# Kernel optimization log

Hardware: AMD Instinct MI355X
Metric: run time of the kernel (lower is better)

Reference implementation:

```python
import jax, jax.numpy as jnp
import numpy as np

N_NODES = 100000
N_EDGES = 1600000
NUM_FEATURES = 512
HIDDEN = 128
NUM_CLASSES = 40


def setup_inputs() -> dict:
    key = jax.random.key(0)
    ks = jax.random.split(key, 6)
    x = jax.random.normal(ks[0], (N_NODES, NUM_FEATURES), dtype=jnp.float32)
    edge_index = jax.random.randint(ks[1], (2, N_EDGES), 0, N_NODES, dtype=jnp.int32)
    W1 = jax.random.normal(ks[2], (NUM_FEATURES, HIDDEN), dtype=jnp.float32) * 0.05
    b1 = jnp.zeros((HIDDEN,), dtype=jnp.float32)
    W2 = jax.random.normal(ks[3], (HIDDEN, NUM_CLASSES), dtype=jnp.float32) * 0.05
    b2 = jnp.zeros((NUM_CLASSES,), dtype=jnp.float32)
    return {"x": x, "edge_index": edge_index, "W1": W1, "b1": b1, "W2": W2, "b2": b2}


def _gcn_conv(x, W, b, src, dst, n):
    # PyG GCNConv: h = W x; out = D^{-1/2} (A + I) D^{-1/2} h + b
    h = x @ W                                            # [N, out]
    deg = jax.ops.segment_sum(jnp.ones(src.shape[0], h.dtype), dst,
                              num_segments=n) + 1.0      # +1 for self loop
    inv_sqrt = jax.lax.rsqrt(deg)                        # [N]
    coef = inv_sqrt[src] * inv_sqrt[dst]                 # [E]
    msgs = h[src] * coef[:, None]                        # [E, out] gather
    agg = jax.ops.segment_sum(msgs, dst, num_segments=n) # scatter-add
    agg = agg + h * (inv_sqrt * inv_sqrt)[:, None]       # self-loop term
    return agg + b


def reference(x, edge_index, W1, b1, W2, b2):
    src, dst = edge_index[0], edge_index[1]
    n = x.shape[0]
    h = jax.nn.relu(_gcn_conv(x, W1, b1, src, dst, n))
    # F.dropout(training=self.training): eval mode -> identity
    out = _gcn_conv(h, W2, b2, src, dst, n)
    return jax.nn.log_softmax(out, axis=1)
```

## Files before the change

kernel.cpp:

```cpp
#include <hip/hip_runtime.h>
#include <hip/hip_bf16.h>
#include <math.h>

#define N_NODES 100000
#define N_EDGES 1600000
#define F_IN 512
#define HID 128
#define NCLS 40

typedef __attribute__((ext_vector_type(8))) short short8;
typedef __attribute__((ext_vector_type(4))) float floatx4;

__device__ __forceinline__ unsigned short f2bf(float x) {
    unsigned u = __builtin_bit_cast(unsigned, x);
    unsigned r = (u + 0x7FFFu + ((u >> 16) & 1u)) >> 16;
    return (unsigned short)r;
}
__device__ __forceinline__ float bflo(unsigned u) {
    return __builtin_bit_cast(float, u << 16);
}
__device__ __forceinline__ float bfhi(unsigned u) {
    return __builtin_bit_cast(float, u & 0xFFFF0000u);
}


__global__ void k_zero_int(int* p, int n) {
    int i = blockIdx.x * blockDim.x + threadIdx.x;
    if (i < n) p[i] = 0;
}


__global__ void k_count_deg(const int* __restrict__ dst, int* __restrict__ deg, int e) {
    int i = blockIdx.x * blockDim.x + threadIdx.x;
    if (i < e) atomicAdd(&deg[dst[i]], 1);
}


#define SCAN_B 256

__global__ __launch_bounds__(SCAN_B) void k_scan1(const int* __restrict__ deg,
                                                  int* __restrict__ rp,
                                                  int* __restrict__ bsums,
                                                  float* __restrict__ inv, int n) {
    __shared__ int s[SCAN_B];
    int tid = threadIdx.x;
    int i = blockIdx.x * SCAN_B + tid;
    int v = (i < n) ? deg[i] : 0;
    if (i < n) inv[i] = rsqrtf((float)v + 1.0f);
    s[tid] = v;
    __syncthreads();
    for (int off = 1; off < SCAN_B; off <<= 1) {
        int t = (tid >= off) ? s[tid - off] : 0;
        __syncthreads();
        s[tid] += t;
        __syncthreads();
    }
    if (i < n) rp[i] = s[tid] - v;
    if (tid == SCAN_B - 1) bsums[blockIdx.x] = s[tid];
}

__global__ __launch_bounds__(512) void k_scan2(int* __restrict__ bsums, int nb) {
    __shared__ int s[512];
    int tid = threadIdx.x;
    int v = (tid < nb) ? bsums[tid] : 0;
    s[tid] = v;
    __syncthreads();
    for (int off = 1; off < 512; off <<= 1) {
        int t = (tid >= off) ? s[tid - off] : 0;
        __syncthreads();
        s[tid] += t;
        __syncthreads();
    }
    if (tid < nb) bsums[tid] = s[tid] - v;
}

__global__ void k_scan3(int* __restrict__ rp, const int* __restrict__ bsums, int n) {
    int i = blockIdx.x * SCAN_B + threadIdx.x;
    if (i < n) rp[i] += bsums[blockIdx.x];
}


__global__ void k_fill(const int* __restrict__ src, const int* __restrict__ dst,
                       const int* __restrict__ rp, int* __restrict__ cursor,
                       int* __restrict__ csr_src, int e) {
    int i = blockIdx.x * blockDim.x + threadIdx.x;
    if (i >= e) return;
    int d = dst[i];
    int pos = atomicAdd(&cursor[d], 1);
    csr_src[rp[d] + pos] = src[i];
}


__global__ __launch_bounds__(256) void k_w1t(const float* __restrict__ W1,
                                             unsigned short* __restrict__ W1t) {
    int idx = blockIdx.x * 256 + threadIdx.x;
    int n = idx >> 9, k = idx & 511;
    W1t[idx] = f2bf(W1[k * HID + n]);
}


__global__ __launch_bounds__(256) void k_w2prep(const float* __restrict__ W2,
                                                unsigned short* __restrict__ W2th,
                                                unsigned short* __restrict__ W2tl) {
    int idx = blockIdx.x * 256 + threadIdx.x;
    int n = idx >> 7, k = idx & 127;
    float v = (n < NCLS) ? W2[k * NCLS + n] : 0.f;
    unsigned short hi = f2bf(v);
    unsigned short lo = f2bf(v - bflo(hi));
    W2th[idx] = hi;
    W2tl[idx] = lo;
}


#define GM 128

__global__ __launch_bounds__(256) void k_gemm1_mfma(
    const float* __restrict__ A,
    const unsigned short* __restrict__ Bt,
    const float* __restrict__ inv,
    unsigned short* __restrict__ C,
    int M)
{
    __shared__ unsigned short Asl[128 * 40];
    __shared__ unsigned short Bsl[128 * 40];

    const int tid  = threadIdx.x;
    const int wave = tid >> 6;
    const int lane = tid & 63;
    const int quad = lane >> 4;
    const int l15  = lane & 15;
    const int wm   = (wave >> 1) * 64;
    const int wn   = (wave & 1) * 64;
    const int block_m = blockIdx.x * GM;

    floatx4 acc[4][4];
    #pragma unroll
    for (int i = 0; i < 4; ++i)
        #pragma unroll
        for (int j = 0; j < 4; ++j) acc[i][j] = (floatx4){0.f, 0.f, 0.f, 0.f};

    for (int k0 = 0; k0 < F_IN; k0 += 32) {
        #pragma unroll
        for (int i = 0; i < 4; ++i) {
            int f  = tid + 256 * i;
            int r  = f >> 3;
            int kq = f & 7;
            int gr = block_m + r;
            gr = gr < M ? gr : M - 1;
            floatx4 v = *(const floatx4*)&A[(size_t)gr * F_IN + k0 + kq * 4];
            unsigned lo = (unsigned)f2bf(v.x) | ((unsigned)f2bf(v.y) << 16);
            unsigned hi = (unsigned)f2bf(v.z) | ((unsigned)f2bf(v.w) << 16);
            *(uint2*)&Asl[r * 40 + kq * 4] = make_uint2(lo, hi);
        }
        #pragma unroll
        for (int i = 0; i < 2; ++i) {
            int f  = tid + 256 * i;
            int r  = f >> 2;
            int kq = f & 3;
            int4 v = *(const int4*)&Bt[(size_t)r * F_IN + k0 + kq * 8];
            *(int4*)&Bsl[r * 40 + kq * 8] = v;
        }
        __syncthreads();

        short8 af[4], bf[4];
        #pragma unroll
        for (int t = 0; t < 4; ++t)
            af[t] = *(const short8*)&Asl[(wm + t * 16 + l15) * 40 + quad * 8];
        #pragma unroll
        for (int t = 0; t < 4; ++t)
            bf[t] = *(const short8*)&Bsl[(wn + t * 16 + l15) * 40 + quad * 8];

        #pragma unroll
        for (int tm = 0; tm < 4; ++tm)
            #pragma unroll
            for (int tn = 0; tn < 4; ++tn)
                acc[tm][tn] = __builtin_amdgcn_mfma_f32_16x16x32_bf16(
                    af[tm], bf[tn], acc[tm][tn], 0, 0, 0);
        __syncthreads();
    }

    #pragma unroll
    for (int tm = 0; tm < 4; ++tm) {
        #pragma unroll
        for (int r = 0; r < 4; ++r) {
            int row = block_m + wm + tm * 16 + quad * 4 + r;
            if (row < M) {
                float iv = inv[row];
                #pragma unroll
                for (int tn = 0; tn < 4; ++tn)
                    C[(size_t)row * HID + wn + tn * 16 + l15] =
                        f2bf(acc[tm][tn][r] * iv);
            }
        }
    }
}


__global__ __launch_bounds__(256) void k_gather1(
    const unsigned* __restrict__ h1s,
    const int* __restrict__ rp, const int* __restrict__ deg,
    const float* __restrict__ inv, const int* __restrict__ csr_src,
    const float* __restrict__ b1, float* __restrict__ hrelu)
{
    const int wave = threadIdx.x >> 6;
    const int lane = threadIdx.x & 63;
    const int node = blockIdx.x * 4 + wave;
    const int start = rp[node];
    const int cnt = deg[node];

    unsigned u = h1s[(size_t)node * 64 + lane];
    float acc0 = bflo(u), acc1 = bfhi(u);

    int t = 0;
    for (; t + 4 <= cnt; t += 4) {
        int s0 = csr_src[start + t + 0];
        int s1 = csr_src[start + t + 1];
        int s2 = csr_src[start + t + 2];
        int s3 = csr_src[start + t + 3];
        unsigned u0 = h1s[(size_t)s0 * 64 + lane];
        unsigned u1 = h1s[(size_t)s1 * 64 + lane];
        unsigned u2 = h1s[(size_t)s2 * 64 + lane];
        unsigned u3 = h1s[(size_t)s3 * 64 + lane];
        acc0 += (bflo(u0) + bflo(u1)) + (bflo(u2) + bflo(u3));
        acc1 += (bfhi(u0) + bfhi(u1)) + (bfhi(u2) + bfhi(u3));
    }
    for (; t < cnt; ++t) {
        int s = csr_src[start + t];
        unsigned uu = h1s[(size_t)s * 64 + lane];
        acc0 += bflo(uu);
        acc1 += bfhi(uu);
    }

    float invd = inv[node];
    float2 b = *(const float2*)&b1[lane * 2];
    float v0 = fmaxf(acc0 * invd + b.x, 0.f);
    float v1 = fmaxf(acc1 * invd + b.y, 0.f);
    *(float2*)&hrelu[(size_t)node * HID + lane * 2] = make_float2(v0, v1);
}


#define G2M 128

__global__ __launch_bounds__(256) void k_gemm2_mfma(
    const float* __restrict__ H,
    const unsigned short* __restrict__ Bh,
    const unsigned short* __restrict__ Bl,
    const float* __restrict__ inv,
    unsigned short* __restrict__ C,
    int M)
{
    __shared__ unsigned short Ahs[128 * 40];
    __shared__ unsigned short Als[128 * 40];
    __shared__ unsigned short Bhs[48 * 136];
    __shared__ unsigned short Bls[48 * 136];

    const int tid  = threadIdx.x;
    const int wave = tid >> 6;
    const int lane = tid & 63;
    const int quad = lane >> 4;
    const int l15  = lane & 15;
    const int wm   = wave * 32;
    const int block_m = blockIdx.x * G2M;

    for (int i = tid; i < 768; i += 256) {
        int n = i >> 4;
        int k = (i & 15) * 8;
        *(int4*)&Bhs[n * 136 + k] = *(const int4*)&Bh[n * 128 + k];
        *(int4*)&Bls[n * 136 + k] = *(const int4*)&Bl[n * 128 + k];
    }

    floatx4 acc[2][3];
    #pragma unroll
    for (int i = 0; i < 2; ++i)
        #pragma unroll
        for (int j = 0; j < 3; ++j) acc[i][j] = (floatx4){0.f, 0.f, 0.f, 0.f};

    for (int k0 = 0; k0 < HID; k0 += 32) {
        #pragma unroll
        for (int i = 0; i < 4; ++i) {
            int f  = tid + 256 * i;
            int r  = f >> 3;
            int kq = f & 7;
            int gr = block_m + r;
            gr = gr < M ? gr : M - 1;
            floatx4 v = *(const floatx4*)&H[(size_t)gr * HID + k0 + kq * 4];
            unsigned short hx = f2bf(v.x), hy = f2bf(v.y);
            unsigned short hz = f2bf(v.z), hw = f2bf(v.w);
            unsigned short lx = f2bf(v.x - bflo(hx));
            unsigned short ly = f2bf(v.y - bflo(hy));
            unsigned short lz = f2bf(v.z - bflo(hz));
            unsigned short lw = f2bf(v.w - bflo(hw));
            *(uint2*)&Ahs[r * 40 + kq * 4] =
                make_uint2((unsigned)hx | ((unsigned)hy << 16),
                           (unsigned)hz | ((unsigned)hw << 16));
            *(uint2*)&Als[r * 40 + kq * 4] =
                make_uint2((unsigned)lx | ((unsigned)ly << 16),
                           (unsigned)lz | ((unsigned)lw << 16));
        }
        __syncthreads();

        short8 ah[2], al[2], bh[3], bl[3];
        #pragma unroll
        for (int t = 0; t < 2; ++t) {
            ah[t] = *(const short8*)&Ahs[(wm + t * 16 + l15) * 40 + quad * 8];
            al[t] = *(const short8*)&Als[(wm + t * 16 + l15) * 40 + quad * 8];
        }
        #pragma unroll
        for (int t = 0; t < 3; ++t) {
            bh[t] = *(const short8*)&Bhs[(t * 16 + l15) * 136 + k0 + quad * 8];
            bl[t] = *(const short8*)&Bls[(t * 16 + l15) * 136 + k0 + quad * 8];
        }

        #pragma unroll
        for (int tm = 0; tm < 2; ++tm)
            #pragma unroll
            for (int tn = 0; tn < 3; ++tn) {
                acc[tm][tn] = __builtin_amdgcn_mfma_f32_16x16x32_bf16(
                    ah[tm], bh[tn], acc[tm][tn], 0, 0, 0);
                acc[tm][tn] = __builtin_amdgcn_mfma_f32_16x16x32_bf16(
                    al[tm], bh[tn], acc[tm][tn], 0, 0, 0);
                acc[tm][tn] = __builtin_amdgcn_mfma_f32_16x16x32_bf16(
                    ah[tm], bl[tn], acc[tm][tn], 0, 0, 0);
            }
        __syncthreads();
    }

    #pragma unroll
    for (int tm = 0; tm < 2; ++tm) {
        #pragma unroll
        for (int r = 0; r < 4; ++r) {
            int row = block_m + wm + tm * 16 + quad * 4 + r;
            if (row < M) {
                float iv = inv[row];
                #pragma unroll
                for (int tn = 0; tn < 3; ++tn) {
                    int col = tn * 16 + l15;
                    if (col < NCLS)
                        C[(size_t)row * NCLS + col] = f2bf(acc[tm][tn][r] * iv);
                }
            }
        }
    }
}


__global__ __launch_bounds__(256) void k_gather2(
    const unsigned* __restrict__ h2s,
    const int* __restrict__ rp, const int* __restrict__ deg,
    const float* __restrict__ inv, const int* __restrict__ csr_src,
    const float* __restrict__ b2, float* __restrict__ out)
{
    const int wave = threadIdx.x >> 6;
    const int lane = threadIdx.x & 63;
    const int node = blockIdx.x * 4 + wave;
    const int g = lane / 20;
    const int j = lane - g * 20;
    const int start = rp[node];
    const int cnt = deg[node];

    float acc0 = 0.f, acc1 = 0.f;
    if (g == 0) {
        unsigned u = h2s[(size_t)node * 20 + j];
        acc0 = bflo(u);
        acc1 = bfhi(u);
    }
    if (g < 3) {
        int t = g;
        for (; t + 3 < cnt; t += 6) {
            int s0 = csr_src[start + t];
            int s1 = csr_src[start + t + 3];
            unsigned u0 = h2s[(size_t)s0 * 20 + j];
            unsigned u1 = h2s[(size_t)s1 * 20 + j];
            acc0 += bflo(u0) + bflo(u1);
            acc1 += bfhi(u0) + bfhi(u1);
        }
        if (t < cnt) {
            int s = csr_src[start + t];
            unsigned u = h2s[(size_t)s * 20 + j];
            acc0 += bflo(u);
            acc1 += bfhi(u);
        }
    }
    acc0 += __shfl(acc0, j + 20) + __shfl(acc0, j + 40);
    acc1 += __shfl(acc1, j + 20) + __shfl(acc1, j + 40);

    float invd = inv[node];
    float v0 = -INFINITY, v1 = -INFINITY;
    if (g == 0) {
        float2 b = *(const float2*)&b2[j * 2];
        v0 = acc0 * invd + b.x;
        v1 = acc1 * invd + b.y;
    }
    float m = fmaxf(v0, v1);
    #pragma unroll
    for (int mask = 16; mask; mask >>= 1) m = fmaxf(m, __shfl_xor(m, mask));
    float e = (g == 0) ? (__expf(v0 - m) + __expf(v1 - m)) : 0.f;
    #pragma unroll
    for (int mask = 16; mask; mask >>= 1) e += __shfl_xor(e, mask);
    if (g == 0) {
        float lg = __logf(e);
        *(float2*)&out[(size_t)node * NCLS + j * 2] =
            make_float2(v0 - m - lg, v1 - m - lg);
    }
}


extern "C" void kernel_launch(void* const* d_in, const int* in_sizes, int n_in,
                              void* d_out, int out_size, void* d_ws, size_t ws_size,
                              hipStream_t stream) {
    const float* x   = (const float*)d_in[0];
    const int*   ei  = (const int*)d_in[1];
    const float* W1  = (const float*)d_in[2];
    const float* b1  = (const float*)d_in[3];
    const float* W2  = (const float*)d_in[4];
    const float* b2  = (const float*)d_in[5];
    float* out = (float*)d_out;

    const int* src = ei;
    const int* dst = ei + N_EDGES;

    char* wsb = (char*)d_ws;
    float* inv      = (float*)wsb;
    float* slot1    = inv + 131072;
    float* hrelu    = slot1 + (size_t)N_NODES * HID;
    int*   deg      = (int*)(hrelu + (size_t)N_NODES * HID);
    int*   rp       = deg + 131072;
    int*   cursor   = rp + 131072;
    int*   bsums    = cursor + 131072;
    int*   csr_src  = bsums + 1024;
    unsigned short* W2th = (unsigned short*)(csr_src + N_EDGES);
    unsigned short* W2tl = W2th + 48 * 128;
    unsigned short* h1s_st = (unsigned short*)slot1;
    unsigned short* h2s_st = (unsigned short*)slot1;
    unsigned* h1s_ld = (unsigned*)slot1;
    unsigned* h2s_ld = (unsigned*)slot1;
    unsigned short* W1t = (unsigned short*)cursor;

    const int T = 256;
    const int NB = (N_NODES + SCAN_B - 1) / SCAN_B;

    k_zero_int<<<(131072 * 2) / T, T, 0, stream>>>(deg, 131072 * 2);
    k_zero_int<<<131072 / T, T, 0, stream>>>(cursor, 131072);
    k_count_deg<<<N_EDGES / T, T, 0, stream>>>(dst, deg, N_EDGES);

    k_scan1<<<NB, SCAN_B, 0, stream>>>(deg, rp, bsums, inv, N_NODES);
    k_scan2<<<1, 512, 0, stream>>>(bsums, NB);
    k_scan3<<<NB, SCAN_B, 0, stream>>>(rp, bsums, N_NODES);
    k_fill<<<N_EDGES / T, T, 0, stream>>>(src, dst, rp, cursor, csr_src, N_EDGES);

    k_w1t<<<(F_IN * HID) / T, T, 0, stream>>>(W1, W1t);
    k_w2prep<<<(48 * 128) / T, T, 0, stream>>>(W2, W2th, W2tl);

    k_gemm1_mfma<<<(N_NODES + GM - 1) / GM, T, 0, stream>>>(x, W1t, inv, h1s_st, N_NODES);
    k_gather1<<<N_NODES / 4, T, 0, stream>>>(h1s_ld, rp, deg, inv, csr_src, b1, hrelu);

    k_gemm2_mfma<<<(N_NODES + G2M - 1) / G2M, T, 0, stream>>>(hrelu, W2th, W2tl, inv, h2s_st, N_NODES);
    k_gather2<<<N_NODES / 4, T, 0, stream>>>(h2s_ld, rp, deg, inv, csr_src, b2, out);
}
```

Measured before the change: 625.6 us.

## Double-buffer LDS and prefetch global tiles in both GEMM kernels

The first GEMM now uses two LDS buffers and issues the global loads for the next K-slice into registers before running the MFMAs on the current slice. The converted values go to the alternate buffer afterwards, which leaves one barrier per step. The second GEMM prefetches its next H slice into registers after the barrier, so the loads overlap the MFMA work. This is meant to hide global load latency, at the cost of twice the LDS and more registers, which could lower occupancy.

```diff
diff --git a/kernel.cpp b/kernel.cpp
--- a/kernel.cpp
+++ b/kernel.cpp
@@ -121,8 +121,8 @@
     unsigned short* __restrict__ C,
     int M)
 {
-    __shared__ unsigned short Asl[128 * 40];
-    __shared__ unsigned short Bsl[128 * 40];
+    __shared__ unsigned short Asl[2][128 * 40];
+    __shared__ unsigned short Bsl[2][128 * 40];
 
     const int tid  = threadIdx.x;
     const int wave = tid >> 6;
@@ -133,49 +133,85 @@
     const int wn   = (wave & 1) * 64;
     const int block_m = blockIdx.x * GM;
 
+    const int ra = tid >> 3, kqa = tid & 7;
+    const int rb = tid >> 2, kqb = tid & 3;
+
+    size_t aoff[4];
+    #pragma unroll
+    for (int i = 0; i < 4; ++i) {
+        int gr = block_m + ra + 32 * i;
+        gr = gr < M ? gr : M - 1;
+        aoff[i] = (size_t)gr * F_IN + kqa * 4;
+    }
+    size_t boff[2];
+    #pragma unroll
+    for (int i = 0; i < 2; ++i)
+        boff[i] = (size_t)(rb + 64 * i) * F_IN + kqb * 8;
+
+    floatx4 areg[4];
+    int4 breg[2];
+
     floatx4 acc[4][4];
     #pragma unroll
     for (int i = 0; i < 4; ++i)
         #pragma unroll
         for (int j = 0; j < 4; ++j) acc[i][j] = (floatx4){0.f, 0.f, 0.f, 0.f};
 
-    for (int k0 = 0; k0 < F_IN; k0 += 32) {
-        #pragma unroll
-        for (int i = 0; i < 4; ++i) {
-            int f  = tid + 256 * i;
-            int r  = f >> 3;
-            int kq = f & 7;
-            int gr = block_m + r;
-            gr = gr < M ? gr : M - 1;
-            floatx4 v = *(const floatx4*)&A[(size_t)gr * F_IN + k0 + kq * 4];
-            unsigned lo = (unsigned)f2bf(v.x) | ((unsigned)f2bf(v.y) << 16);
-            unsigned hi = (unsigned)f2bf(v.z) | ((unsigned)f2bf(v.w) << 16);
-            *(uint2*)&Asl[r * 40 + kq * 4] = make_uint2(lo, hi);
-        }
-        #pragma unroll
-        for (int i = 0; i < 2; ++i) {
-            int f  = tid + 256 * i;
-            int r  = f >> 2;
-            int kq = f & 3;
-            int4 v = *(const int4*)&Bt[(size_t)r * F_IN + k0 + kq * 8];
-            *(int4*)&Bsl[r * 40 + kq * 8] = v;
-        }
-        __syncthreads();
-
-        short8 af[4], bf[4];
+    #pragma unroll
+    for (int i = 0; i < 4; ++i) areg[i] = *(const floatx4*)&A[aoff[i]];
+    #pragma unroll
+    for (int i = 0; i < 2; ++i) breg[i] = *(const int4*)&Bt[boff[i]];
+    #pragma unroll
+    for (int i = 0; i < 4; ++i) {
+        floatx4 v = areg[i];
+        unsigned lo = (unsigned)f2bf(v.x) | ((unsigned)f2bf(v.y) << 16);
+        unsigned hi = (unsigned)f2bf(v.z) | ((unsigned)f2bf(v.w) << 16);
+        *(uint2*)&Asl[0][(ra + 32 * i) * 40 + kqa * 4] = make_uint2(lo, hi);
+    }
+    #pragma unroll
+    for (int i = 0; i < 2; ++i)
+        *(int4*)&Bsl[0][(rb + 64 * i) * 40 + kqb * 8] = breg[i];
+    __syncthreads();
+
+    #pragma unroll 2
+    for (int step = 0; step < 16; ++step) {
+        const int buf = step & 1;
+
+        if (step < 15) {
+            const int k1 = (step + 1) * 32;
+            #pragma unroll
+            for (int i = 0; i < 4; ++i) areg[i] = *(const floatx4*)&A[aoff[i] + k1];
+            #pragma unroll
+            for (int i = 0; i < 2; ++i) breg[i] = *(const int4*)&Bt[boff[i] + k1];
+        }
+
+        short8 af[4], bfr[4];
         #pragma unroll
         for (int t = 0; t < 4; ++t)
-            af[t] = *(const short8*)&Asl[(wm + t * 16 + l15) * 40 + quad * 8];
+            af[t] = *(const short8*)&Asl[buf][(wm + t * 16 + l15) * 40 + quad * 8];
         #pragma unroll
         for (int t = 0; t < 4; ++t)
-            bf[t] = *(const short8*)&Bsl[(wn + t * 16 + l15) * 40 + quad * 8];
+            bfr[t] = *(const short8*)&Bsl[buf][(wn + t * 16 + l15) * 40 + quad * 8];
 
         #pragma unroll
         for (int tm = 0; tm < 4; ++tm)
             #pragma unroll
             for (int tn = 0; tn < 4; ++tn)
                 acc[tm][tn] = __builtin_amdgcn_mfma_f32_16x16x32_bf16(
-                    af[tm], bf[tn], acc[tm][tn], 0, 0, 0);
+                    af[tm], bfr[tn], acc[tm][tn], 0, 0, 0);
+
+        if (step < 15) {
+            #pragma unroll
+            for (int i = 0; i < 4; ++i) {
+                floatx4 v = areg[i];
+                unsigned lo = (unsigned)f2bf(v.x) | ((unsigned)f2bf(v.y) << 16);
+                unsigned hi = (unsigned)f2bf(v.z) | ((unsigned)f2bf(v.w) << 16);
+                *(uint2*)&Asl[buf ^ 1][(ra + 32 * i) * 40 + kqa * 4] = make_uint2(lo, hi);
+            }
+            #pragma unroll
+            for (int i = 0; i < 2; ++i)
+                *(int4*)&Bsl[buf ^ 1][(rb + 64 * i) * 40 + kqb * 8] = breg[i];
+        }
         __syncthreads();
     }
 
@@ -269,36 +305,51 @@
         *(int4*)&Bls[n * 136 + k] = *(const int4*)&Bl[n * 128 + k];
     }
 
+    const int ra = tid >> 3, kqa = tid & 7;
+    size_t aoff[4];
+    #pragma unroll
+    for (int i = 0; i < 4; ++i) {
+        int gr = block_m + ra + 32 * i;
+        gr = gr < M ? gr : M - 1;
+        aoff[i] = (size_t)gr * HID + kqa * 4;
+    }
+
+    floatx4 hreg[4];
+    #pragma unroll
+    for (int i = 0; i < 4; ++i) hreg[i] = *(const floatx4*)&H[aoff[i]];
+
     floatx4 acc[2][3];
     #pragma unroll
     for (int i = 0; i < 2; ++i)
         #pragma unroll
         for (int j = 0; j < 3; ++j) acc[i][j] = (floatx4){0.f, 0.f, 0.f, 0.f};
 
-    for (int k0 = 0; k0 < HID; k0 += 32) {
+    for (int step = 0; step < 4; ++step) {
         #pragma unroll
         for (int i = 0; i < 4; ++i) {
-            int f  = tid + 256 * i;
-            int r  = f >> 3;
-            int kq = f & 7;
-            int gr = block_m + r;
-            gr = gr < M ? gr : M - 1;
-            floatx4 v = *(const floatx4*)&H[(size_t)gr * HID + k0 + kq * 4];
+            floatx4 v = hreg[i];
             unsigned short hx = f2bf(v.x), hy = f2bf(v.y);
             unsigned short hz = f2bf(v.z), hw = f2bf(v.w);
             unsigned short lx = f2bf(v.x - bflo(hx));
             unsigned short ly = f2bf(v.y - bflo(hy));
             unsigned short lz = f2bf(v.z - bflo(hz));
             unsigned short lw = f2bf(v.w - bflo(hw));
-            *(uint2*)&Ahs[r * 40 + kq * 4] =
+            *(uint2*)&Ahs[(ra + 32 * i) * 40 + kqa * 4] =
                 make_uint2((unsigned)hx | ((unsigned)hy << 16),
                            (unsigned)hz | ((unsigned)hw << 16));
-            *(uint2*)&Als[r * 40 + kq * 4] =
+            *(uint2*)&Als[(ra + 32 * i) * 40 + kqa * 4] =
                 make_uint2((unsigned)lx | ((unsigned)ly << 16),
                            (unsigned)lz | ((unsigned)lw << 16));
         }
         __syncthreads();
 
+        if (step < 3) {
+            const int k1 = (step + 1) * 32;
+            #pragma unroll
+            for (int i = 0; i < 4; ++i) hreg[i] = *(const floatx4*)&H[aoff[i] + k1];
+        }
+
+        const int k0 = step * 32;
         short8 ah[2], al[2], bh[3], bl[3];
         #pragma unroll
         for (int t = 0; t < 2; ++t) {
```

Result: no change. 623.3 us (-0.4%).
